# Performance work log

Measured on AMD Instinct MI355X. Metric: run time of the kernel, lower is better.

Reference implementation:

```python
import jax, jax.numpy as jnp
import numpy as np
import math

D = 384; N = 1024; BATCH = 8
D_STATE = 64; D_CONV = 4; EXPAND = 2
D_INNER = EXPAND * D
DT_RANK = math.ceil(D / 16)
W_WIN = 4; N_HEADS = 4; HEAD_DIM = D // N_HEADS
BOTTLENECK = max(8, D // 4)

def _perms(n):
    side = int(math.isqrt(n))
    p0 = np.arange(n)
    p1 = np.arange(n).reshape(side, side).T.reshape(-1)   # column-major
    p2 = p0[::-1].copy()                                   # reverse horizontal
    p3 = p1[::-1].copy()                                   # reverse vertical
    return [jnp.asarray(p) for p in (p0, p1, p2, p3)]

PERMS = _perms(N)

def layernorm(x, w, b, eps=1e-5):
    mu = jnp.mean(x, -1, keepdims=True)
    var = jnp.var(x, -1, keepdims=True)
    return (x - mu) * jax.lax.rsqrt(var + eps) * w + b

def mamba(x, in_proj_w, conv_w, conv_b, x_proj_w, dt_proj_w, dt_proj_b, A_log, D_skip, out_proj_w):
    # canonical pure-python Mamba block (selective scan SSM)
    B, L, _ = x.shape
    xz = x @ in_proj_w.T                      # [B,L,2*di]
    xin, z = jnp.split(xz, 2, axis=-1)
    xc = jnp.swapaxes(xin, 1, 2)              # [B,di,L]
    xc = jax.lax.conv_general_dilated(xc, conv_w, (1,), [(D_CONV - 1, 0)], feature_group_count=D_INNER)
    u = jax.nn.silu(jnp.swapaxes(xc + conv_b[None, :, None], 1, 2))  # [B,L,di]
    x_dbl = u @ x_proj_w.T                    # [B,L,dt_rank+2*ds]
    dt, Bm, Cm = jnp.split(x_dbl, [DT_RANK, DT_RANK + D_STATE], axis=-1)
    dt = jax.nn.softplus(dt @ dt_proj_w.T + dt_proj_b)  # [B,L,di]
    A = -jnp.exp(A_log)                       # [di,ds]
    def step(h, inp):
        dt_t, B_t, C_t, u_t = inp             # [B,di],[B,ds],[B,ds],[B,di]
        dA = jnp.exp(dt_t[:, :, None] * A[None])
        h = dA * h + dt_t[:, :, None] * B_t[:, None, :] * u_t[:, :, None]
        y = jnp.einsum('bds,bs->bd', h, C_t)
        return h, y
    h0 = jnp.zeros((B, D_INNER, D_STATE), x.dtype)
    xs = (jnp.swapaxes(dt, 0, 1), jnp.swapaxes(Bm, 0, 1), jnp.swapaxes(Cm, 0, 1), jnp.swapaxes(u, 0, 1))
    _, ys = jax.lax.scan(step, h0, xs)
    y = jnp.swapaxes(ys, 0, 1) + u * D_skip
    return (y * jax.nn.silu(z)) @ out_proj_w.T

def local_attn(x, qkv_w, qkv_b, ao_w, ao_b):
    # sliding-window MHA over windows of W_WIN tokens (N % W_WIN == 0 here, no pad)
    B, Nn, Dd = x.shape
    xw = x.reshape(B * (Nn // W_WIN), W_WIN, Dd)
    qkv = xw @ qkv_w.T + qkv_b
    q, k, v = jnp.split(qkv, 3, axis=-1)
    def heads(t):
        return t.reshape(t.shape[0], W_WIN, N_HEADS, HEAD_DIM).transpose(0, 2, 1, 3)
    q, k, v = heads(q), heads(k), heads(v)
    scores = jnp.einsum('bhqd,bhkd->bhqk', q, k) / math.sqrt(HEAD_DIM)
    attn = jax.nn.softmax(scores, axis=-1)
    o = jnp.einsum('bhqk,bhkd->bhqd', attn, v).transpose(0, 2, 1, 3).reshape(-1, W_WIN, Dd)
    return (o @ ao_w.T + ao_b).reshape(B, Nn, Dd)

def setup_inputs() -> dict:
    key = jax.random.key(0)
    ks = jax.random.split(key, 16)
    def rn(k, shape, scale=0.02):
        return jax.random.normal(k, shape, jnp.float32) * scale
    return dict(
        x=jax.random.normal(ks[0], (BATCH, N, D), jnp.float32),
        r_w1=rn(ks[1], (BOTTLENECK, D)), r_b1=jnp.zeros((BOTTLENECK,), jnp.float32),
        r_w2=rn(ks[2], (4, BOTTLENECK)), r_b2=jnp.zeros((4,), jnp.float32),
        ln1_w=jnp.ones((D,), jnp.float32), ln1_b=jnp.zeros((D,), jnp.float32),
        ln2_w=jnp.ones((D,), jnp.float32), ln2_b=jnp.zeros((D,), jnp.float32),
        in_proj_w=rn(ks[3], (2 * D_INNER, D)),
        conv_w=rn(ks[4], (D_INNER, 1, D_CONV), 0.1), conv_b=jnp.zeros((D_INNER,), jnp.float32),
        x_proj_w=rn(ks[5], (DT_RANK + 2 * D_STATE, D_INNER)),
        dt_proj_w=rn(ks[6], (D_INNER, DT_RANK), 0.1),
        dt_proj_b=jnp.full((D_INNER,), -3.0, jnp.float32) + rn(ks[7], (D_INNER,), 0.1),
        A_log=jnp.log(jnp.tile(jnp.arange(1, D_STATE + 1, dtype=jnp.float32), (D_INNER, 1))),
        D_skip=jnp.ones((D_INNER,), jnp.float32),
        out_proj_w=rn(ks[8], (D, D_INNER)),
        qkv_w=rn(ks[9], (3 * D, D)), qkv_b=jnp.zeros((3 * D,), jnp.float32),
        ao_w=rn(ks[10], (D, D)), ao_b=jnp.zeros((D,), jnp.float32),
        gate=jnp.full((1,), 0.1, jnp.float32),
        lng_w=jnp.ones((D,), jnp.float32), lng_b=jnp.zeros((D,), jnp.float32),
    )

def reference(x, r_w1, r_b1, r_w2, r_b2, ln1_w, ln1_b, ln2_w, ln2_b,
              in_proj_w, conv_w, conv_b, x_proj_w, dt_proj_w, dt_proj_b,
              A_log, D_skip, out_proj_w, qkv_w, qkv_b, ao_w, ao_b,
              gate, lng_w, lng_b):
    # ScanRouter: mean-pool -> MLP -> softmax over 4 directions (dropout=eval)
    g = jnp.mean(x, axis=1)
    h = jax.nn.gelu(g @ r_w1.T + r_b1, approximate=False)
    w = jax.nn.softmax(h @ r_w2.T + r_b2, axis=-1)   # [B,4]
    xn = layernorm(x, ln1_w, ln1_b)
    fused = jnp.zeros_like(x)
    for d in range(4):
        out = mamba(xn[:, PERMS[d], :], in_proj_w, conv_w, conv_b, x_proj_w,
                    dt_proj_w, dt_proj_b, A_log, D_skip, out_proj_w)
        fused = fused + w[:, d, None, None] * out
    x = x + fused                                    # residual (dropout=eval)
    xn2 = layernorm(x, ln2_w, ln2_b)
    ao = local_attn(xn2, qkv_w, qkv_b, ao_w, ao_b)
    return layernorm(xn2 + gate * ao, lng_w, lng_b)
```

## Files before the change

kernel.cpp:

```cpp
#include <hip/hip_runtime.h>
#include <math.h>


#define NSEQ  1024
#define DMODEL 384
#define DINNER 768
#define DSTATE 64
#define XW 152
#define SCHUNK 128

typedef unsigned short u16;
typedef __attribute__((ext_vector_type(8))) short short8;
typedef __attribute__((ext_vector_type(4))) float f32x4;

__device__ __forceinline__ float bf2f(u16 u){
  union { unsigned int i; float f; } c; c.i = ((unsigned int)u) << 16; return c.f;
}
__device__ __forceinline__ u16 f2bf(float f){
  union { float f; unsigned int i; } c; c.f = f;
  unsigned int x = c.i;
  return (u16)((x + 0x7fffu + ((x >> 16) & 1u)) >> 16);
}
__device__ __forceinline__ float4 unp4(uint2 u){
  float4 f;
  f.x = bf2f((u16)(u.x & 0xffffu)); f.y = bf2f((u16)(u.x >> 16));
  f.z = bf2f((u16)(u.y & 0xffffu)); f.w = bf2f((u16)(u.y >> 16));
  return f;
}

template<int DIR>
__device__ __forceinline__ int permi(int i){
  if (DIR == 0) return i;
  if (DIR == 1) return ((i & 31) << 5) | (i >> 5);
  if (DIR == 2) return 1023 - i;
  int j = 1023 - i; return ((j & 31) << 5) | (j >> 5);
}

__global__ __launch_bounds__(384) void router_mean_kernel(const float* __restrict__ X, float* __restrict__ G){
  int b = blockIdx.y, chunk = blockIdx.x, c = threadIdx.x;
  float s = 0.f;
  const float* xp = X + ((size_t)b*NSEQ + (size_t)chunk*64)*DMODEL + c;
  for (int l = 0; l < 64; ++l) s += xp[(size_t)l*DMODEL];
  atomicAdd(&G[b*DMODEL + c], s * (1.f/1024.f));
}

__global__ __launch_bounds__(96) void router_mlp_kernel(const float* __restrict__ G,
    const float* __restrict__ w1, const float* __restrict__ b1,
    const float* __restrict__ w2, const float* __restrict__ b2, float* __restrict__ WR){
  int b = blockIdx.x, j = threadIdx.x;
  __shared__ float hs[96];
  __shared__ float ls[4];
  float a = b1[j];
  const float* g = G + b*DMODEL;
  for (int c = 0; c < DMODEL; ++c) a += g[c] * w1[j*DMODEL + c];
  hs[j] = 0.5f * a * (1.f + erff(a * 0.70710678118654752f));
  __syncthreads();
  if (j < 4) {
    float lg = b2[j];
    for (int jj = 0; jj < 96; ++jj) lg += hs[jj] * w2[j*96 + jj];
    ls[j] = lg;
  }
  __syncthreads();
  if (j == 0) {
    float mx = fmaxf(fmaxf(ls[0],ls[1]),fmaxf(ls[2],ls[3]));
    float e0=__expf(ls[0]-mx), e1=__expf(ls[1]-mx), e2=__expf(ls[2]-mx), e3=__expf(ls[3]-mx);
    float s = e0+e1+e2+e3;
    WR[b*4+0]=e0/s; WR[b*4+1]=e1/s; WR[b*4+2]=e2/s; WR[b*4+3]=e3/s;
  }
}

__global__ __launch_bounds__(256) void ln_bf16out_kernel(const float* __restrict__ X,
    const float* __restrict__ w, const float* __restrict__ bb, u16* __restrict__ O){
  int row = blockIdx.x*4 + (threadIdx.x >> 6);
  int lane = threadIdx.x & 63;
  const float* xr = X + (size_t)row*DMODEL;
  float v[6]; float s=0.f, s2=0.f;
  #pragma unroll
  for (int j=0;j<6;++j){ float t = xr[lane + j*64]; v[j]=t; s+=t; s2+=t*t; }
  #pragma unroll
  for (int m=1;m<64;m<<=1){ s += __shfl_xor(s,m,64); s2 += __shfl_xor(s2,m,64); }
  float mu = s*(1.f/DMODEL);
  float rs = rsqrtf(s2*(1.f/DMODEL) - mu*mu + 1e-5f);
  u16* o = O + (size_t)row*DMODEL;
  #pragma unroll
  for (int j=0;j<6;++j){ int i = lane+j*64; o[i] = f2bf((v[j]-mu)*rs*w[i] + bb[i]); }
}

__global__ __launch_bounds__(256) void ln_kernel(const float* __restrict__ X,
    const float* __restrict__ w, const float* __restrict__ bb, float* __restrict__ O){
  int row = blockIdx.x*4 + (threadIdx.x >> 6);
  int lane = threadIdx.x & 63;
  const float* xr = X + (size_t)row*DMODEL;
  float v[6]; float s=0.f, s2=0.f;
  #pragma unroll
  for (int j=0;j<6;++j){ float t = xr[lane + j*64]; v[j]=t; s+=t; s2+=t*t; }
  #pragma unroll
  for (int m=1;m<64;m<<=1){ s += __shfl_xor(s,m,64); s2 += __shfl_xor(s2,m,64); }
  float mu = s*(1.f/DMODEL);
  float rs = rsqrtf(s2*(1.f/DMODEL) - mu*mu + 1e-5f);
  float* o = O + (size_t)row*DMODEL;
  #pragma unroll
  for (int j=0;j<6;++j){ int i = lane+j*64; o[i] = (v[j]-mu)*rs*w[i] + bb[i]; }
}

__global__ __launch_bounds__(256) void ln_final_kernel(const float* __restrict__ XN2,
    const float* __restrict__ AO, const float* __restrict__ gatep,
    const float* __restrict__ w, const float* __restrict__ bb, float* __restrict__ OUT){
  int row = blockIdx.x*4 + (threadIdx.x >> 6);
  int lane = threadIdx.x & 63;
  float gate = gatep[0];
  const float* xr = XN2 + (size_t)row*DMODEL;
  const float* ar = AO + (size_t)row*DMODEL;
  float v[6]; float s=0.f, s2=0.f;
  #pragma unroll
  for (int j=0;j<6;++j){ int i = lane+j*64; float t = xr[i] + gate*ar[i]; v[j]=t; s+=t; s2+=t*t; }
  #pragma unroll
  for (int m=1;m<64;m<<=1){ s += __shfl_xor(s,m,64); s2 += __shfl_xor(s2,m,64); }
  float mu = s*(1.f/DMODEL);
  float rs = rsqrtf(s2*(1.f/DMODEL) - mu*mu + 1e-5f);
  float* o = OUT + (size_t)row*DMODEL;
  #pragma unroll
  for (int j=0;j<6;++j){ int i = lane+j*64; o[i] = (v[j]-mu)*rs*w[i] + bb[i]; }
}

__global__ __launch_bounds__(256) void cvt4_kernel(const float* __restrict__ src,
    u16* __restrict__ dst, int n4){
  int i = blockIdx.x*256 + threadIdx.x;
  if (i >= n4) return;
  float4 v = ((const float4*)src)[i];
  ushort4 o; o.x=f2bf(v.x); o.y=f2bf(v.y); o.z=f2bf(v.z); o.w=f2bf(v.w);
  ((ushort4*)dst)[i] = o;
}

__global__ __launch_bounds__(256) void mgemm_kernel(
    const u16* __restrict__ A, int lda,
    const u16* __restrict__ W, int K, int N,
    const float* __restrict__ bias,
    const float* __restrict__ resid,
    int act,
    int obf,
    void* __restrict__ C, int ldc)
{
  const int lane = threadIdx.x & 63;
  const int wv = threadIdx.x >> 6;
  const int m0 = (blockIdx.y*4 + wv) * 64;
  const int n0 = blockIdx.x * 64;
  const int r  = lane & 15;
  const int kg = lane >> 4;
  f32x4 acc[4][4];
  #pragma unroll
  for (int i=0;i<4;++i){
    #pragma unroll
    for (int j=0;j<4;++j) acc[i][j] = (f32x4)0.f;
  }
  for (int k0 = 0; k0 < K; k0 += 32) {
    const bool kval = (k0 + kg*8) < K;
    short8 a[4], b[4];
    #pragma unroll
    for (int i = 0; i < 4; ++i) {
      a[i] = kval ? *(const short8*)(A + (size_t)(m0 + i*16 + r)*lda + k0 + kg*8) : (short8)0;
      int n = n0 + i*16 + r;
      b[i] = (kval && n < N) ? *(const short8*)(W + (size_t)n*K + k0 + kg*8) : (short8)0;
    }
    #pragma unroll
    for (int ai = 0; ai < 4; ++ai)
      #pragma unroll
      for (int bi = 0; bi < 4; ++bi)
        acc[ai][bi] = __builtin_amdgcn_mfma_f32_16x16x32_bf16(a[ai], b[bi], acc[ai][bi], 0, 0, 0);
  }
  #pragma unroll
  for (int ai = 0; ai < 4; ++ai) {
    int mrow = m0 + ai*16 + kg*4;
    #pragma unroll
    for (int bi = 0; bi < 4; ++bi) {
      int n = n0 + bi*16 + r;
      if (n < N) {
        #pragma unroll
        for (int q = 0; q < 4; ++q) {
          float v = acc[ai][bi][q];
          int m = mrow + q;
          if (bias) v += bias[n];
          if (act == 1) v = (v > 20.f) ? v : log1pf(__expf(v));
          if (resid) v += resid[(size_t)m*ldc + n];
          if (obf) ((u16*)C)[(size_t)m*ldc + n] = f2bf(v);
          else     ((float*)C)[(size_t)m*ldc + n] = v;
        }
      }
    }
  }
}

__global__ __launch_bounds__(256) void zsilu_kernel(u16* __restrict__ XZ){
  int idx = blockIdx.x*256 + threadIdx.x;
  int row = idx / 96, q = idx % 96;
  u16* p = XZ + (size_t)row*1536 + DINNER + q*8;
  uint4 v = *(uint4*)p;
  unsigned w0=v.x, w1=v.y, w2=v.z, w3=v.w;
  #define ZS(w) { \
    float lo = bf2f((u16)((w) & 0xffffu)); \
    float hi = bf2f((u16)((w) >> 16)); \
    lo = lo / (1.f + __expf(-lo)); \
    hi = hi / (1.f + __expf(-hi)); \
    (w) = (unsigned)f2bf(lo) | ((unsigned)f2bf(hi) << 16); }
  ZS(w0) ZS(w1) ZS(w2) ZS(w3)
  #undef ZS
  v.x=w0; v.y=w1; v.z=w2; v.w=w3;
  *(uint4*)p = v;
}

template<int DIR>
__global__ __launch_bounds__(256) void conv_silu_kernel(const u16* __restrict__ XZ,
    const float* __restrict__ cw, const float* __restrict__ cb, u16* __restrict__ Uo){
  int idx = blockIdx.x*256 + threadIdx.x;
  int c = idx % DINNER;
  int rest = idx / DINNER;
  int i = rest & 1023;
  int b = rest >> 10;
  float acc = cb[c];
  #pragma unroll
  for (int k = 0; k < 4; ++k) {
    int ii = i - 3 + k;
    if (ii >= 0)
      acc += cw[c*4 + k] * bf2f(XZ[((size_t)b*NSEQ + permi<DIR>(ii))*1536 + c]);
  }
  Uo[idx] = f2bf(acc / (1.f + __expf(-acc)));
}

template<int CTRL>
__device__ __forceinline__ float dpp_add(float v){
  int t = __builtin_amdgcn_update_dpp(0, __float_as_int(v), CTRL, 0xf, 0xf, true);
  return v + __int_as_float(t);
}
__device__ __forceinline__ float row16_sum(float p){
  p = dpp_add<0x128>(p);
  p = dpp_add<0x124>(p);
  p = dpp_add<0x122>(p);
  p = dpp_add<0x121>(p);
  return p;
}

template<int DIR>
__device__ __forceinline__ void scan_body(
    const u16* __restrict__ xd, const u16* __restrict__ dt0,
    const u16* __restrict__ u0, const u16* __restrict__ z0,
    u16* __restrict__ ob,
    float* __restrict__ lacc,
    const float* __restrict__ A_log, const float* __restrict__ Dskip,
    float wgt, int c0w, int grp)
{
  const int lane = threadIdx.x & 63;
  const int g = lane >> 4;
  const int q = lane & 15;
  const int c = c0w + g;
  const float4 Alq = *(const float4*)(A_log + (size_t)c*DSTATE + q*4);
  const float As0 = -__expf(Alq.x), As1 = -__expf(Alq.y);
  const float As2 = -__expf(Alq.z), As3 = -__expf(Alq.w);
  const float dsk = Dskip[c];
  const u16* dtp = dt0 + c;
  const u16* up  = u0 + c;
  const u16* zp  = z0 + DINNER + c;
  float* lw = lacc + DIR*SCHUNK*8 + grp*4 + g;

#define SLOAD(k, l) { int lr = (l) < 1023 ? (l) : 1023;                     \
    const u16* x2 = xd + (size_t)lr*XW;                                     \
    uint2 bd = *(const uint2*)(x2 + 24 + q*4);                              \
    uint2 cd = *(const uint2*)(x2 + 88 + q*4);                              \
    B##k = unp4(bd); C##k = unp4(cd);                                       \
    t##k = bf2f(dtp[(size_t)lr*DINNER]);                                    \
    u##k = bf2f(up [(size_t)lr*DINNER]);                                    \
    z##k = bf2f(zp [(size_t)permi<DIR>(lr)*1536]); }

#define SSTEP(k, l) {                                                       \
    float dtu = t##k * u##k;                                                \
    float e0 = __expf(t##k*As0), e1 = __expf(t##k*As1);                     \
    float e2 = __expf(t##k*As2), e3 = __expf(t##k*As3);                     \
    h0 = e0*h0 + dtu*B##k.x; h1 = e1*h1 + dtu*B##k.y;                       \
    h2 = e2*h2 + dtu*B##k.z; h3 = e3*h3 + dtu*B##k.w;                       \
    float p = h0*C##k.x + h1*C##k.y + h2*C##k.z + h3*C##k.w;                \
    p = row16_sum(p);                                                       \
    float o = wgt*(p + u##k*dsk)*z##k;                                      \
    if (q == 0) lw[((l)&(SCHUNK-1))*8] = o; }

  float4 B0,C0,B1,C1,B2,C2,B3,C3;
  float t0,u0_,z0_, t1,u1,z1, t2,u2,z2, t3,u3,z3;
  #define u0 u0_
  #define z0 z0_
  float h0=0.f, h1=0.f, h2=0.f, h3=0.f;
  SLOAD(0,0) SLOAD(1,1) SLOAD(2,2) SLOAD(3,3)
  __builtin_amdgcn_sched_barrier(0);
  for (int l0 = 0; l0 < NSEQ; l0 += SCHUNK) {
    for (int l = l0; l < l0 + SCHUNK; l += 4) {
      SSTEP(0,l)   SLOAD(0,l+4) __builtin_amdgcn_sched_barrier(0);
      SSTEP(1,l+1) SLOAD(1,l+5) __builtin_amdgcn_sched_barrier(0);
      SSTEP(2,l+2) SLOAD(2,l+6) __builtin_amdgcn_sched_barrier(0);
      SSTEP(3,l+3) SLOAD(3,l+7) __builtin_amdgcn_sched_barrier(0);
    }
    __syncthreads();
    for (int i = threadIdx.x; i < SCHUNK*8; i += 512) {
      float s = lacc[i] + lacc[SCHUNK*8 + i] + lacc[2*SCHUNK*8 + i] + lacc[3*SCHUNK*8 + i];
      int row = i >> 3, cc = i & 7;
      ob[(size_t)(l0 + row)*DINNER + cc] = f2bf(s);
    }
    __syncthreads();
  }
#undef u0
#undef z0
#undef SLOAD
#undef SSTEP
}

__global__ __launch_bounds__(512) void scan_all_kernel(
    const u16* __restrict__ XD4, const u16* __restrict__ DT4,
    const u16* __restrict__ U4, const u16* __restrict__ XZ,
    u16* __restrict__ OB,
    const float* __restrict__ A_log, const float* __restrict__ Dskip,
    const float* __restrict__ WR, int b0, int BS)
{
  __shared__ float lacc[4*SCHUNK*8];
  const int bx = blockIdx.x;
  const int sx = (bx & 7)*12 + (bx >> 3);
  const int c0 = sx * 8;
  const int b = blockIdx.y;
  const int w = threadIdx.x >> 6;
  const int dir = w & 3;
  const int grp = w >> 2;
  const int c0w = c0 + grp*4;
  const size_t drb = ((size_t)dir*BS + b) * NSEQ;
  const u16* xd = XD4 + drb*XW;
  const u16* dt = DT4 + drb*DINNER;
  const u16* uu = U4  + drb*DINNER;
  const u16* zz = XZ  + (size_t)b*NSEQ*1536;
  u16* ob = OB + (size_t)b*NSEQ*DINNER + c0;
  const float wgt = WR[(b0+b)*4 + dir];
  switch (dir) {
    case 0: scan_body<0>(xd, dt, uu, zz, ob, lacc, A_log, Dskip, wgt, c0w, grp); break;
    case 1: scan_body<1>(xd, dt, uu, zz, ob, lacc, A_log, Dskip, wgt, c0w, grp); break;
    case 2: scan_body<2>(xd, dt, uu, zz, ob, lacc, A_log, Dskip, wgt, c0w, grp); break;
    default: scan_body<3>(xd, dt, uu, zz, ob, lacc, A_log, Dskip, wgt, c0w, grp); break;
  }
}

__global__ __launch_bounds__(256) void attn_kernel(const float* __restrict__ QKV, float* __restrict__ O){
  int idx = blockIdx.x*256 + threadIdx.x;
  int tq = idx & 3, h = (idx >> 2) & 3, w = idx >> 4;
  size_t row0 = (size_t)w * 4;
  const float4* qp = (const float4*)(QKV + (row0 + tq)*1152 + h*96);
  float sc[4];
  #pragma unroll
  for (int tk = 0; tk < 4; ++tk) {
    const float4* kp = (const float4*)(QKV + (row0 + tk)*1152 + 384 + h*96);
    float d = 0.f;
    #pragma unroll
    for (int j = 0; j < 24; ++j) {
      float4 qf = qp[j], kf = kp[j];
      d += qf.x*kf.x + qf.y*kf.y + qf.z*kf.z + qf.w*kf.w;
    }
    sc[tk] = d * 0.10206207261596575f;
  }
  float mx = fmaxf(fmaxf(sc[0],sc[1]),fmaxf(sc[2],sc[3]));
  float s = 0.f;
  #pragma unroll
  for (int tk=0;tk<4;++tk){ sc[tk]=__expf(sc[tk]-mx); s+=sc[tk]; }
  float inv = 1.f/s;
  #pragma unroll
  for (int tk=0;tk<4;++tk) sc[tk]*=inv;
  float4* op = (float4*)(O + (row0 + tq)*DMODEL + h*96);
  #pragma unroll 4
  for (int j = 0; j < 24; ++j) {
    float4 o = {0.f,0.f,0.f,0.f};
    #pragma unroll
    for (int tk=0;tk<4;++tk){
      const float4* vp = (const float4*)(QKV + (row0+tk)*1152 + 768 + h*96);
      float4 vf = vp[j];
      o.x += sc[tk]*vf.x; o.y += sc[tk]*vf.y; o.z += sc[tk]*vf.z; o.w += sc[tk]*vf.w;
    }
    op[j] = o;
  }
}

extern "C" void kernel_launch(void* const* d_in, const int* in_sizes, int n_in,
                              void* d_out, int out_size, void* d_ws, size_t ws_size,
                              hipStream_t stream)
{
  (void)in_sizes; (void)n_in; (void)out_size;
  const float* x         = (const float*)d_in[0];
  const float* r_w1      = (const float*)d_in[1];
  const float* r_b1      = (const float*)d_in[2];
  const float* r_w2      = (const float*)d_in[3];
  const float* r_b2      = (const float*)d_in[4];
  const float* ln1_w     = (const float*)d_in[5];
  const float* ln1_b     = (const float*)d_in[6];
  const float* ln2_w     = (const float*)d_in[7];
  const float* ln2_b     = (const float*)d_in[8];
  const float* in_proj_w = (const float*)d_in[9];
  const float* conv_w    = (const float*)d_in[10];
  const float* conv_b    = (const float*)d_in[11];
  const float* x_proj_w  = (const float*)d_in[12];
  const float* dt_proj_w = (const float*)d_in[13];
  const float* dt_proj_b = (const float*)d_in[14];
  const float* A_log     = (const float*)d_in[15];
  const float* D_skip    = (const float*)d_in[16];
  const float* out_proj_w= (const float*)d_in[17];
  const float* qkv_w     = (const float*)d_in[18];
  const float* qkv_b     = (const float*)d_in[19];
  const float* ao_w      = (const float*)d_in[20];
  const float* ao_b      = (const float*)d_in[21];
  const float* gate      = (const float*)d_in[22];
  const float* lng_w     = (const float*)d_in[23];
  const float* lng_b     = (const float*)d_in[24];

  float* ws = (float*)d_ws;
  float* WR = ws;
  float* G  = ws + 64;
  u16*  WBF = (u16*)(ws + 3200);
  u16* ipw = WBF + 0;
  u16* xpw = WBF + 589824;
  u16* dtw = WBF + 706560;
  u16* opw = WBF + 724992;
  u16* qkw = WBF + 1019904;
  u16* aow = WBF + 1462272;

  int BS = 8;
  while (BS > 1) {
    size_t need = ((size_t)808064 + (size_t)BS*1024*5296) * sizeof(float);
    if (need <= ws_size) break;
    BS >>= 1;
  }
  const int R = BS * 1024;

  (void)hipMemsetAsync(ws, 0, 4096*sizeof(float), stream);
  router_mean_kernel<<<dim3(16,8),384,0,stream>>>(x, G);
  router_mlp_kernel<<<8,96,0,stream>>>(G, r_w1, r_b1, r_w2, r_b2, WR);

  cvt4_kernel<<<576,256,0,stream>>>(in_proj_w, ipw, 147456);
  cvt4_kernel<<<114,256,0,stream>>>(x_proj_w,  xpw, 29184);
  cvt4_kernel<<<18,256,0,stream>>>(dt_proj_w,  dtw, 4608);
  cvt4_kernel<<<288,256,0,stream>>>(out_proj_w,opw, 73728);
  cvt4_kernel<<<432,256,0,stream>>>(qkv_w,     qkw, 110592);
  cvt4_kernel<<<144,256,0,stream>>>(ao_w,      aow, 36864);

  float* base = ws + 808064;
  u16*   ABF  = (u16*)base;
  u16*   XZbf = (u16*)(base + (size_t)R*384);
  u16*   Ub4  = (u16*)(base + (size_t)R*1152);
  u16*   XD4  = (u16*)(base + (size_t)R*2688);
  u16*   DT4  = (u16*)(base + (size_t)R*2992);
  float* XN2  = base + (size_t)R*4528;
  float* AOb  = base + (size_t)R*4912;
  float* X2   = (float*)Ub4;
  float* QKV  = (float*)Ub4 + (size_t)R*384;
  float* ATTO = (float*)DT4;

  for (int s = 0; s < 8/BS; ++s) {
    const int b0 = s * BS;
    const size_t xoff = (size_t)b0 * NSEQ * DMODEL;

    ln_bf16out_kernel<<<R/4,256,0,stream>>>(x + xoff, ln1_w, ln1_b, ABF);
    mgemm_kernel<<<dim3(24,R/256),256,0,stream>>>(ABF,384, ipw,384,1536, nullptr,nullptr,0,1, XZbf,1536);
    zsilu_kernel<<<(R*96)/256,256,0,stream>>>(XZbf);
    conv_silu_kernel<0><<<3*R,256,0,stream>>>(XZbf, conv_w, conv_b, Ub4);
    conv_silu_kernel<1><<<3*R,256,0,stream>>>(XZbf, conv_w, conv_b, Ub4 + (size_t)R*768);
    conv_silu_kernel<2><<<3*R,256,0,stream>>>(XZbf, conv_w, conv_b, Ub4 + (size_t)2*R*768);
    conv_silu_kernel<3><<<3*R,256,0,stream>>>(XZbf, conv_w, conv_b, Ub4 + (size_t)3*R*768);
    mgemm_kernel<<<dim3(3,R/64),256,0,stream>>>(Ub4,768, xpw,768,152, nullptr,nullptr,0,1, XD4,152);
    mgemm_kernel<<<dim3(12,R/64),256,0,stream>>>(XD4,152, dtw,24,768, dt_proj_b,nullptr,1,1, DT4,768);
    scan_all_kernel<<<dim3(96,BS),512,0,stream>>>(XD4, DT4, Ub4, XZbf, ABF, A_log, D_skip, WR, b0, BS);
    mgemm_kernel<<<dim3(6,R/256),256,0,stream>>>(ABF,768, opw,768,384, nullptr,x + xoff,0,0, X2,384);
    ln_kernel<<<R/4,256,0,stream>>>(X2, ln2_w, ln2_b, XN2);
    cvt4_kernel<<<(R*96)/256,256,0,stream>>>(XN2, ABF, R*96);
    mgemm_kernel<<<dim3(18,R/256),256,0,stream>>>(ABF,384, qkw,384,1152, qkv_b,nullptr,0,0, QKV,1152);
    attn_kernel<<<R/64,256,0,stream>>>(QKV, ATTO);
    cvt4_kernel<<<(R*96)/256,256,0,stream>>>(ATTO, ABF, R*96);
    mgemm_kernel<<<dim3(6,R/256),256,0,stream>>>(ABF,384, aow,384,384, ao_b,nullptr,0,0, AOb,384);
    ln_final_kernel<<<R/4,256,0,stream>>>(XN2, AOb, gate, lng_w, lng_b, (float*)d_out + xoff);
  }
}
```

Before: 1.114 ms.

## Interleave u and dt per row, merge conv launches, fuse bf16 casts

The four per-direction conv+silu launches become one grid with a direction axis. Its output goes into an interleaved buffer where each row holds u and dt side by side, and the dt projection writes straight into the second half. The scan then reads u and dt from one row through incrementing pointers, and steps the z index incrementally instead of recomputing permutation indices. LayerNorm2 now also emits a bf16 copy, and attention writes bf16 output directly, which removes two cvt kernels. The trade-offs are a wider row stride for the x_proj GEMM input and a changed workspace layout.

```diff
diff --git a/kernel.cpp b/kernel.cpp
--- a/kernel.cpp
+++ b/kernel.cpp
@@ -34,6 +34,13 @@
   if (DIR == 1) return ((i & 31) << 5) | (i >> 5);
   if (DIR == 2) return 1023 - i;
   int j = 1023 - i; return ((j & 31) << 5) | (j >> 5);
+}
+template<int DIR>
+__device__ __forceinline__ int znext(int zi){
+  if (DIR == 0) return zi + 4;
+  if (DIR == 2) return zi - 4;
+  if (DIR == 1) { int t = zi + 128; return (t >= 1024) ? t - 1023 : t; }
+  int t = zi - 128; return (t < 0) ? t + 1023 : t;
 }
 
 __global__ __launch_bounds__(384) void router_mean_kernel(const float* __restrict__ X, float* __restrict__ G){
@@ -86,8 +93,9 @@
   for (int j=0;j<6;++j){ int i = lane+j*64; o[i] = f2bf((v[j]-mu)*rs*w[i] + bb[i]); }
 }
 
-__global__ __launch_bounds__(256) void ln_kernel(const float* __restrict__ X,
-    const float* __restrict__ w, const float* __restrict__ bb, float* __restrict__ O){
+__global__ __launch_bounds__(256) void ln_dual_kernel(const float* __restrict__ X,
+    const float* __restrict__ w, const float* __restrict__ bb,
+    float* __restrict__ O, u16* __restrict__ OB){
   int row = blockIdx.x*4 + (threadIdx.x >> 6);
   int lane = threadIdx.x & 63;
   const float* xr = X + (size_t)row*DMODEL;
@@ -99,8 +107,9 @@
   float mu = s*(1.f/DMODEL);
   float rs = rsqrtf(s2*(1.f/DMODEL) - mu*mu + 1e-5f);
   float* o = O + (size_t)row*DMODEL;
-  #pragma unroll
-  for (int j=0;j<6;++j){ int i = lane+j*64; o[i] = (v[j]-mu)*rs*w[i] + bb[i]; }
+  u16* ob = OB + (size_t)row*DMODEL;
+  #pragma unroll
+  for (int j=0;j<6;++j){ int i = lane+j*64; float r = (v[j]-mu)*rs*w[i] + bb[i]; o[i] = r; ob[i] = f2bf(r); }
 }
 
 __global__ __launch_bounds__(256) void ln_final_kernel(const float* __restrict__ XN2,
@@ -209,21 +218,34 @@
 }
 
 template<int DIR>
-__global__ __launch_bounds__(256) void conv_silu_kernel(const u16* __restrict__ XZ,
-    const float* __restrict__ cw, const float* __restrict__ cb, u16* __restrict__ Uo){
+__device__ __forceinline__ float conv_acc(const u16* __restrict__ XZ,
+    const float* __restrict__ cw, int b, int i, int c, float acc){
+  #pragma unroll
+  for (int k = 0; k < 4; ++k) {
+    int ii = i - 3 + k;
+    if (ii >= 0)
+      acc += cw[c*4 + k] * bf2f(XZ[((size_t)b*NSEQ + permi<DIR>(ii))*1536 + c]);
+  }
+  return acc;
+}
+
+__global__ __launch_bounds__(256) void conv_silu_all_kernel(const u16* __restrict__ XZ,
+    const float* __restrict__ cw, const float* __restrict__ cb,
+    u16* __restrict__ UD4, int BS){
+  int dir = blockIdx.y;
   int idx = blockIdx.x*256 + threadIdx.x;
   int c = idx % DINNER;
   int rest = idx / DINNER;
   int i = rest & 1023;
   int b = rest >> 10;
   float acc = cb[c];
-  #pragma unroll
-  for (int k = 0; k < 4; ++k) {
-    int ii = i - 3 + k;
-    if (ii >= 0)
-      acc += cw[c*4 + k] * bf2f(XZ[((size_t)b*NSEQ + permi<DIR>(ii))*1536 + c]);
-  }
-  Uo[idx] = f2bf(acc / (1.f + __expf(-acc)));
+  switch (dir) {
+    case 0: acc = conv_acc<0>(XZ, cw, b, i, c, acc); break;
+    case 1: acc = conv_acc<1>(XZ, cw, b, i, c, acc); break;
+    case 2: acc = conv_acc<2>(XZ, cw, b, i, c, acc); break;
+    default: acc = conv_acc<3>(XZ, cw, b, i, c, acc); break;
+  }
+  UD4[((size_t)(dir*BS + b)*NSEQ + i)*1536 + c] = f2bf(acc / (1.f + __expf(-acc)));
 }
 
 template<int CTRL>
@@ -241,8 +263,8 @@
 
 template<int DIR>
 __device__ __forceinline__ void scan_body(
-    const u16* __restrict__ xd, const u16* __restrict__ dt0,
-    const u16* __restrict__ u0, const u16* __restrict__ z0,
+    const u16* __restrict__ xd, const u16* __restrict__ ud,
+    const u16* __restrict__ zb,
     u16* __restrict__ ob,
     float* __restrict__ lacc,
     const float* __restrict__ A_log, const float* __restrict__ Dskip,
@@ -256,19 +278,26 @@
   const float As0 = -__expf(Alq.x), As1 = -__expf(Alq.y);
   const float As2 = -__expf(Alq.z), As3 = -__expf(Alq.w);
   const float dsk = Dskip[c];
-  const u16* dtp = dt0 + c;
-  const u16* up  = u0 + c;
-  const u16* zp  = z0 + DINNER + c;
+  const u16* zp = zb + DINNER + c;
   float* lw = lacc + DIR*SCHUNK*8 + grp*4 + g;
 
-#define SLOAD(k, l) { int lr = (l) < 1023 ? (l) : 1023;                     \
-    const u16* x2 = xd + (size_t)lr*XW;                                     \
-    uint2 bd = *(const uint2*)(x2 + 24 + q*4);                              \
-    uint2 cd = *(const uint2*)(x2 + 88 + q*4);                              \
+  const u16* px0 = xd + 0*XW + 24 + q*4;
+  const u16* px1 = xd + 1*XW + 24 + q*4;
+  const u16* px2 = xd + 2*XW + 24 + q*4;
+  const u16* px3 = xd + 3*XW + 24 + q*4;
+  const u16* pu0 = ud + 0*1536 + c;
+  const u16* pu1 = ud + 1*1536 + c;
+  const u16* pu2 = ud + 2*1536 + c;
+  const u16* pu3 = ud + 3*1536 + c;
+  int zi0 = permi<DIR>(0), zi1 = permi<DIR>(1), zi2 = permi<DIR>(2), zi3 = permi<DIR>(3);
+
+#define SLOAD(k) {                                                          \
+    uint2 bd = *(const uint2*)px##k;                                        \
+    uint2 cd = *(const uint2*)(px##k + 64);                                 \
     B##k = unp4(bd); C##k = unp4(cd);                                       \
-    t##k = bf2f(dtp[(size_t)lr*DINNER]);                                    \
-    u##k = bf2f(up [(size_t)lr*DINNER]);                                    \
-    z##k = bf2f(zp [(size_t)permi<DIR>(lr)*1536]); }
+    u##k = bf2f(pu##k[0]); t##k = bf2f(pu##k[768]);                         \
+    z##k = bf2f(zp[(ptrdiff_t)zi##k * 1536]);                               \
+    px##k += 4*XW; pu##k += 4*1536; zi##k = znext<DIR>(zi##k); }
 
 #define SSTEP(k, l) {                                                       \
     float dtu = t##k * u##k;                                                \
@@ -282,18 +311,16 @@
     if (q == 0) lw[((l)&(SCHUNK-1))*8] = o; }
 
   float4 B0,C0,B1,C1,B2,C2,B3,C3;
-  float t0,u0_,z0_, t1,u1,z1, t2,u2,z2, t3,u3,z3;
-  #define u0 u0_
-  #define z0 z0_
+  float t0,u0,z0, t1,u1,z1, t2,u2,z2, t3,u3,z3;
   float h0=0.f, h1=0.f, h2=0.f, h3=0.f;
-  SLOAD(0,0) SLOAD(1,1) SLOAD(2,2) SLOAD(3,3)
+  SLOAD(0) SLOAD(1) SLOAD(2) SLOAD(3)
   __builtin_amdgcn_sched_barrier(0);
   for (int l0 = 0; l0 < NSEQ; l0 += SCHUNK) {
     for (int l = l0; l < l0 + SCHUNK; l += 4) {
-      SSTEP(0,l)   SLOAD(0,l+4) __builtin_amdgcn_sched_barrier(0);
-      SSTEP(1,l+1) SLOAD(1,l+5) __builtin_amdgcn_sched_barrier(0);
-      SSTEP(2,l+2) SLOAD(2,l+6) __builtin_amdgcn_sched_barrier(0);
-      SSTEP(3,l+3) SLOAD(3,l+7) __builtin_amdgcn_sched_barrier(0);
+      SSTEP(0,l)   SLOAD(0) __builtin_amdgcn_sched_barrier(0);
+      SSTEP(1,l+1) SLOAD(1) __builtin_amdgcn_sched_barrier(0);
+      SSTEP(2,l+2) SLOAD(2) __builtin_amdgcn_sched_barrier(0);
+      SSTEP(3,l+3) SLOAD(3) __builtin_amdgcn_sched_barrier(0);
     }
     __syncthreads();
     for (int i = threadIdx.x; i < SCHUNK*8; i += 512) {
@@ -303,16 +330,13 @@
     }
     __syncthreads();
   }
-#undef u0
-#undef z0
 #undef SLOAD
 #undef SSTEP
 }
 
 __global__ __launch_bounds__(512) void scan_all_kernel(
-    const u16* __restrict__ XD4, const u16* __restrict__ DT4,
-    const u16* __restrict__ U4, const u16* __restrict__ XZ,
-    u16* __restrict__ OB,
+    const u16* __restrict__ XD4, const u16* __restrict__ UD4,
+    const u16* __restrict__ XZ, u16* __restrict__ OB,
     const float* __restrict__ A_log, const float* __restrict__ Dskip,
     const float* __restrict__ WR, int b0, int BS)
 {
@@ -327,20 +351,19 @@
   const int c0w = c0 + grp*4;
   const size_t drb = ((size_t)dir*BS + b) * NSEQ;
   const u16* xd = XD4 + drb*XW;
-  const u16* dt = DT4 + drb*DINNER;
-  const u16* uu = U4  + drb*DINNER;
+  const u16* ud = UD4 + drb*1536;
   const u16* zz = XZ  + (size_t)b*NSEQ*1536;
   u16* ob = OB + (size_t)b*NSEQ*DINNER + c0;
   const float wgt = WR[(b0+b)*4 + dir];
   switch (dir) {
-    case 0: scan_body<0>(xd, dt, uu, zz, ob, lacc, A_log, Dskip, wgt, c0w, grp); break;
-    case 1: scan_body<1>(xd, dt, uu, zz, ob, lacc, A_log, Dskip, wgt, c0w, grp); break;
-    case 2: scan_body<2>(xd, dt, uu, zz, ob, lacc, A_log, Dskip, wgt, c0w, grp); break;
-    default: scan_body<3>(xd, dt, uu, zz, ob, lacc, A_log, Dskip, wgt, c0w, grp); break;
-  }
-}
-
-__global__ __launch_bounds__(256) void attn_kernel(const float* __restrict__ QKV, float* __restrict__ O){
+    case 0: scan_body<0>(xd, ud, zz, ob, lacc, A_log, Dskip, wgt, c0w, grp); break;
+    case 1: scan_body<1>(xd, ud, zz, ob, lacc, A_log, Dskip, wgt, c0w, grp); break;
+    case 2: scan_body<2>(xd, ud, zz, ob, lacc, A_log, Dskip, wgt, c0w, grp); break;
+    default: scan_body<3>(xd, ud, zz, ob, lacc, A_log, Dskip, wgt, c0w, grp); break;
+  }
+}
+
+__global__ __launch_bounds__(256) void attn_kernel(const float* __restrict__ QKV, u16* __restrict__ O){
   int idx = blockIdx.x*256 + threadIdx.x;
   int tq = idx & 3, h = (idx >> 2) & 3, w = idx >> 4;
   size_t row0 = (size_t)w * 4;
@@ -364,7 +387,7 @@
   float inv = 1.f/s;
   #pragma unroll
   for (int tk=0;tk<4;++tk) sc[tk]*=inv;
-  float4* op = (float4*)(O + (row0 + tq)*DMODEL + h*96);
+  u16* op = O + (row0 + tq)*DMODEL + h*96;
   #pragma unroll 4
   for (int j = 0; j < 24; ++j) {
     float4 o = {0.f,0.f,0.f,0.f};
@@ -374,7 +397,8 @@
       float4 vf = vp[j];
       o.x += sc[tk]*vf.x; o.y += sc[tk]*vf.y; o.z += sc[tk]*vf.z; o.w += sc[tk]*vf.w;
     }
-    op[j] = o;
+    ushort4 ov; ov.x=f2bf(o.x); ov.y=f2bf(o.y); ov.z=f2bf(o.z); ov.w=f2bf(o.w);
+    *(ushort4*)(op + j*4) = ov;
   }
 }
 
@@ -442,14 +466,13 @@
   float* base = ws + 808064;
   u16*   ABF  = (u16*)base;
   u16*   XZbf = (u16*)(base + (size_t)R*384);
-  u16*   Ub4  = (u16*)(base + (size_t)R*1152);
-  u16*   XD4  = (u16*)(base + (size_t)R*2688);
-  u16*   DT4  = (u16*)(base + (size_t)R*2992);
+  u16*   UD4  = (u16*)(base + (size_t)R*1152);
+  u16*   XD4  = (u16*)(base + (size_t)R*4224);
   float* XN2  = base + (size_t)R*4528;
   float* AOb  = base + (size_t)R*4912;
-  float* X2   = (float*)Ub4;
-  float* QKV  = (float*)Ub4 + (size_t)R*384;
-  float* ATTO = (float*)DT4;
+  float* X2   = (float*)UD4;
+  float* QKV  = (float*)UD4 + (size_t)R*384;
+  u16*   ATTO = (u16*)((float*)UD4 + (size_t)R*1536);
 
   for (int s = 0; s < 8/BS; ++s) {
     const int b0 = s * BS;
@@ -458,20 +481,15 @@
     ln_bf16out_kernel<<<R/4,256,0,stream>>>(x + xoff, ln1_w, ln1_b, ABF);
     mgemm_kernel<<<dim3(24,R/256),256,0,stream>>>(ABF,384, ipw,384,1536, nullptr,nullptr,0,1, XZbf,1536);
     zsilu_kernel<<<(R*96)/256,256,0,stream>>>(XZbf);
-    conv_silu_kernel<0><<<3*R,256,0,stream>>>(XZbf, conv_w, conv_b, Ub4);
-    conv_silu_kernel<1><<<3*R,256,0,stream>>>(XZbf, conv_w, conv_b, Ub4 + (size_t)R*768);
-    conv_silu_kernel<2><<<3*R,256,0,stream>>>(XZbf, conv_w, conv_b, Ub4 + (size_t)2*R*768);
-    conv_silu_kernel<3><<<3*R,256,0,stream>>>(XZbf, conv_w, conv_b, Ub4 + (size_t)3*R*768);
-    mgemm_kernel<<<dim3(3,R/64),256,0,stream>>>(Ub4,768, xpw,768,152, nullptr,nullptr,0,1, XD4,152);
-    mgemm_kernel<<<dim3(12,R/64),256,0,stream>>>(XD4,152, dtw,24,768, dt_proj_b,nullptr,1,1, DT4,768);
-    scan_all_kernel<<<dim3(96,BS),512,0,stream>>>(XD4, DT4, Ub4, XZbf, ABF, A_log, D_skip, WR, b0, BS);
+    conv_silu_all_kernel<<<dim3(3*R,4),256,0,stream>>>(XZbf, conv_w, conv_b, UD4, BS);
+    mgemm_kernel<<<dim3(3,R/64),256,0,stream>>>(UD4,1536, xpw,768,152, nullptr,nullptr,0,1, XD4,152);
+    mgemm_kernel<<<dim3(12,R/64),256,0,stream>>>(XD4,152, dtw,24,768, dt_proj_b,nullptr,1,1, UD4+768,1536);
+    scan_all_kernel<<<dim3(96,BS),512,0,stream>>>(XD4, UD4, XZbf, ABF, A_log, D_skip, WR, b0, BS);
     mgemm_kernel<<<dim3(6,R/256),256,0,stream>>>(ABF,768, opw,768,384, nullptr,x + xoff,0,0, X2,384);
-    ln_kernel<<<R/4,256,0,stream>>>(X2, ln2_w, ln2_b, XN2);
-    cvt4_kernel<<<(R*96)/256,256,0,stream>>>(XN2, ABF, R*96);
+    ln_dual_kernel<<<R/4,256,0,stream>>>(X2, ln2_w, ln2_b, XN2, ABF);
     mgemm_kernel<<<dim3(18,R/256),256,0,stream>>>(ABF,384, qkw,384,1152, qkv_b,nullptr,0,0, QKV,1152);
     attn_kernel<<<R/64,256,0,stream>>>(QKV, ATTO);
-    cvt4_kernel<<<(R*96)/256,256,0,stream>>>(ATTO, ABF, R*96);
-    mgemm_kernel<<<dim3(6,R/256),256,0,stream>>>(ABF,384, aow,384,384, ao_b,nullptr,0,0, AOb,384);
+    mgemm_kernel<<<dim3(6,R/256),256,0,stream>>>(ATTO,384, aow,384,384, ao_b,nullptr,0,0, AOb,384);
     ln_final_kernel<<<R/4,256,0,stream>>>(XN2, AOb, gate, lng_w, lng_b, (float*)d_out + xoff);
   }
 }
```

After: 1.089 ms. 2.2% less time.
